# Kernel optimization log

Hardware: AMD Instinct MI355X
Metric: run time of the kernel (lower is better)

## Reference

```python
import jax, jax.numpy as jnp
import numpy as np

B, L, D, HW = 128, 512, 512, 512
NEG = -1e9


def _ff(x, weights):
    # feed-forward chain: relu(x @ W) per layer
    for w in weights:
        x = jax.nn.relu(jnp.matmul(x, w))
    return x


def _masked_softmax_flat(logits, mask):
    # softmax over the flattened last axis, masked entries excluded
    logits = jnp.where(mask > 0, logits, NEG)
    return jax.nn.softmax(logits, axis=-1)


def setup_inputs() -> dict:
    key = jax.random.key(0)
    ks = jax.random.split(key, 11)
    u = lambda k, shape: jax.random.uniform(k, shape, jnp.float32, -0.05, 0.05)
    return {
        "premise": jax.random.normal(ks[0], (B, L, D), jnp.float32),
        "hypothesis": jax.random.normal(ks[1], (B, L, D), jnp.float32),
        "premise_mask": jax.random.randint(ks[2], (B, L), 0, 2, jnp.int32),
        "hypothesis_mask": jax.random.randint(ks[3], (B, L), 0, 2, jnp.int32),
        "attend_w0": u(ks[4], (D, HW)),
        "attend_w1": u(ks[5], (HW, HW)),
        "compare_w0": u(ks[6], (2 * D, HW)),
        "compare_w1": u(ks[7], (HW, HW)),
        "aggregate_w0": u(ks[8], (2 * HW, HW)),
        "aggregate_w1": u(ks[9], (HW, HW)),
        "scorer": u(ks[10], (HW, 2)),
    }


def reference(premise, hypothesis, premise_mask, hypothesis_mask,
              attend_w0, attend_w1, compare_w0, compare_w1,
              aggregate_w0, aggregate_w1, scorer):
    pm = premise_mask.astype(premise.dtype)      # [B, P]
    hm = hypothesis_mask.astype(hypothesis.dtype)  # [B, H]
    p_emb = premise * pm[..., None]              # zero out masked words
    h_emb = hypothesis * hm[..., None]

    # Attend: project with shared F, score all pairs
    proj_p = _ff(p_emb, [attend_w0, attend_w1])  # [B, P, HW]
    proj_h = _ff(h_emb, [attend_w0, attend_w1])  # [B, H, HW]
    att = jnp.einsum('bpd,bhd->bph', proj_p, proj_h)  # [B, P, H]
    Bn, P, H = att.shape

    # Faithful to original: softmax over the *flattened* P*H axis with pairwise mask
    p2h_mask = (pm[:, :, None] * hm[:, None, :]).reshape(Bn, P * H)
    h2p_mask = (hm[:, :, None] * pm[:, None, :]).reshape(Bn, H * P)
    p2h = _masked_softmax_flat(att.reshape(Bn, P * H), p2h_mask).reshape(Bn, P, H)
    h2p = _masked_softmax_flat(jnp.swapaxes(att, 1, 2).reshape(Bn, H * P), h2p_mask).reshape(Bn, H, P)

    # Weighted sums (alignments)
    p2h_align = jnp.einsum('bph,bhd->bpd', p2h, h_emb)  # [B, P, D]
    h2p_align = jnp.einsum('bhp,bpd->bhd', h2p, p_emb)  # [B, H, D]

    # Compare with shared G
    compared_p = _ff(jnp.concatenate([p_emb, p2h_align], axis=-1), [compare_w0, compare_w1])
    compared_h = _ff(jnp.concatenate([h_emb, h2p_align], axis=-1), [compare_w0, compare_w1])

    # Aggregate with H, then score
    aggregated = jnp.concatenate([compared_p.sum(axis=1), compared_h.sum(axis=1)], axis=-1)  # [B, 2*HW]
    hidden = _ff(aggregated, [aggregate_w0, aggregate_w1])  # [B, HW]
    return jax.nn.softmax(jnp.matmul(hidden, scorer), axis=-1)  # [B, 2]
```

## Files before the change

kernel.cpp:

```cpp
#include <hip/hip_runtime.h>
#include <hip/hip_bf16.h>
#include <stdint.h>

typedef unsigned short u16;
typedef uint8_t u8;
typedef __bf16 bf16x8 __attribute__((ext_vector_type(8)));
typedef float f32x4 __attribute__((ext_vector_type(4)));

__device__ __forceinline__ u16 f2b(float f){
  uint32_t u = __float_as_uint(f);
  u = (u + 0x7fffu + ((u >> 16) & 1u)) >> 16;
  return (u16)u;
}
__device__ __forceinline__ float b2f(u16 u){
  return __uint_as_float(((uint32_t)u) << 16);
}
__device__ __forceinline__ uint32_t f2e4(float f){
  uint32_t u = __float_as_uint(f);
  uint32_t s = (u >> 24) & 0x80u;
  uint32_t a = u & 0x7fffffffu;
  if (a >= 0x43e00000u) return s | 0x7eu;
  if (a < 0x3c800000u){
    float v = __uint_as_float(a) * 512.0f + 12582912.0f;
    return s | (__float_as_uint(v) & 7u);
  }
  uint32_t t = a - (120u << 23);
  t += 0x7ffffu + ((t >> 20) & 1u);
  return s | (t >> 20);
}
__device__ __forceinline__ u16 e4b(uint32_t b){
  uint32_t s = (b & 0x80u) << 8;
  uint32_t e = (b >> 3) & 15u, m = b & 7u;
  if (e) return (u16)(s | ((e + 120u) << 7) | (m << 4));
  return (u16)(s | f2b((float)m * 0.001953125f));
}

typedef const void __attribute__((address_space(1))) gv_t;
typedef void __attribute__((address_space(3))) sv_t;

__device__ __forceinline__ void gload16(const void* g, void* l){
  __builtin_amdgcn_global_load_lds((gv_t*)g, (sv_t*)l, 16, 0, 0);
}

__global__ __launch_bounds__(256) void cnt_scan(const int* __restrict__ pm,
    const int* __restrict__ hm, int* __restrict__ pfx, int* __restrict__ cnts)
{
  int bs = blockIdx.x;
  const int* msk = (bs < 128) ? pm + bs*512 : hm + (bs-128)*512;
  __shared__ int sA[256], sB[256], fl[512];
  int t = threadIdx.x;
  int a = (msk[2*t] != 0), b = (msk[2*t+1] != 0);
  fl[2*t] = a; fl[2*t+1] = b;
  sA[t] = a + b;
  __syncthreads();
  int* cur = sA; int* nxt = sB;
  #pragma unroll
  for (int off = 1; off < 256; off <<= 1){
    int v = cur[t] + ((t >= off) ? cur[t-off] : 0);
    nxt[t] = v;
    __syncthreads();
    int* tmp = cur; cur = nxt; nxt = tmp;
  }
  int incl = cur[t];
  int excl = incl - fl[2*t] - fl[2*t+1];
  pfx[bs*512 + 2*t]     = excl;
  pfx[bs*512 + 2*t + 1] = excl + fl[2*t];
  if (t == 255) cnts[bs] = incl;
}

__global__ __launch_bounds__(256) void gscan_k(const int* __restrict__ cnts,
    int* __restrict__ gpfx, int* __restrict__ hloc)
{
  __shared__ int sA[256], sB[256];
  int t = threadIdx.x;
  int v0 = cnts[t];
  sA[t] = v0;
  __syncthreads();
  int* cur = sA; int* nxt = sB;
  #pragma unroll
  for (int off = 1; off < 256; off <<= 1){
    int v = cur[t] + ((t >= off) ? cur[t-off] : 0);
    nxt[t] = v;
    __syncthreads();
    int* tmp = cur; cur = nxt; nxt = tmp;
  }
  int incl = cur[t];
  gpfx[t] = incl - v0;
  if (t == 255) gpfx[256] = incl;
  __syncthreads();
  if (t >= 128) hloc[t - 128] = (incl - v0) - cur[127];
}

__global__ __launch_bounds__(256) void compact_copy(
    const float* __restrict__ prem, const float* __restrict__ hyp,
    const int* __restrict__ pm, const int* __restrict__ hm,
    const int* __restrict__ pfx, const int* __restrict__ gpfx,
    u8* __restrict__ embC8, int* __restrict__ rowMap)
{
  int blk = blockIdx.x;
  int bs = blk >> 2, qtr = blk & 3;
  const float* src = (bs < 128) ? prem + (long)bs*262144 : hyp + (long)(bs-128)*262144;
  const int*  msk = (bs < 128) ? pm + bs*512 : hm + (bs-128)*512;
  const int*  pf  = pfx + bs*512;
  long gbase = gpfx[bs];
  int t = threadIdx.x;
  for (int idx = t; idx < 128*32; idx += 256){
    int r = qtr*128 + (idx >> 5);
    if (msk[r] == 0) continue;
    int c = (idx & 31) * 16;
    int dr = pf[r];
    long g = gbase + dr;
    if ((idx & 31) == 0) rowMap[g] = bs*512 + dr;
    const float4* s4 = (const float4*)(src + (long)r*512 + c);
    float4 v0 = s4[0], v1 = s4[1], v2 = s4[2], v3 = s4[3];
    union { u8 o[16]; uint4 q; } u;
    u.o[0]=f2e4(v0.x); u.o[1]=f2e4(v0.y); u.o[2]=f2e4(v0.z); u.o[3]=f2e4(v0.w);
    u.o[4]=f2e4(v1.x); u.o[5]=f2e4(v1.y); u.o[6]=f2e4(v1.z); u.o[7]=f2e4(v1.w);
    u.o[8]=f2e4(v2.x); u.o[9]=f2e4(v2.y); u.o[10]=f2e4(v2.z); u.o[11]=f2e4(v2.w);
    u.o[12]=f2e4(v3.x); u.o[13]=f2e4(v3.y); u.o[14]=f2e4(v3.z); u.o[15]=f2e4(v3.w);
    *(uint4*)&embC8[g*512 + c] = u.q;
  }
}

__global__ void wtrans3_k(const float* __restrict__ W0, const float* __restrict__ W1,
                          const float* __restrict__ W2, u8* __restrict__ O0,
                          u8* __restrict__ O1, u8* __restrict__ O2){
  __shared__ float tile[32][33];
  const float* W = (blockIdx.z == 0) ? W0 : (blockIdx.z == 1 ? W1 : W2);
  u8* out        = (blockIdx.z == 0) ? O0 : (blockIdx.z == 1 ? O1 : O2);
  int c0 = blockIdx.x*32, r0 = blockIdx.y*32;
  int tx = threadIdx.x & 31, ty = threadIdx.x >> 5;
  #pragma unroll
  for (int i = 0; i < 4; ++i){
    int rr = ty + i*8;
    tile[rr][tx] = W[(long)(r0+rr)*512 + c0 + tx];
  }
  __syncthreads();
  #pragma unroll
  for (int i = 0; i < 4; ++i){
    int rr = ty + i*8;
    out[(long)(c0+rr)*512 + r0 + tx] = (u8)f2e4(tile[tx][rr]);
  }
}
__global__ void wtrans_k(const float* __restrict__ W, u8* __restrict__ out, int R, int C){
  __shared__ float tile[32][33];
  int c0 = blockIdx.x*32, r0 = blockIdx.y*32;
  int tx = threadIdx.x & 31, ty = threadIdx.x >> 5;
  #pragma unroll
  for (int i = 0; i < 4; ++i){
    int rr = ty + i*8;
    tile[rr][tx] = W[(long)(r0+rr)*C + c0 + tx];
  }
  __syncthreads();
  #pragma unroll
  for (int i = 0; i < 4; ++i){
    int rr = ty + i*8;
    out[(long)(c0+rr)*R + r0 + tx] = (u8)f2e4(tile[tx][rr]);
  }
}

__global__ __launch_bounds__(256) void btrans2(const u8* __restrict__ in,
    const int* __restrict__ gpfx, const int* __restrict__ cnts,
    u16* __restrict__ outP, u16* __restrict__ outH)
{
  __shared__ u16 tile[64][65];
  int z = blockIdx.z;
  long sbase = (long)gpfx[z] * 512;
  int cnt = cnts[z];
  int r0 = blockIdx.y*64;
  if (r0 >= ((cnt + 31) & ~31)) return;
  u16* dst = (z < 128) ? outP + (long)z*262144 : outH + (long)(z-128)*262144;
  int c0 = blockIdx.x*64;
  int t = threadIdx.x;
  int rr = t >> 3, cc = (t & 7)*8;
  #pragma unroll
  for (int pass = 0; pass < 2; ++pass){
    int r = rr + pass*32;
    uint2 v = {0, 0};
    if (r0 + r < cnt) v = *(const uint2*)&in[sbase + (long)(r0+r)*512 + c0+cc];
    const u8* vv = (const u8*)&v;
    #pragma unroll
    for (int j = 0; j < 8; ++j) tile[r][cc+j] = (r0 + r < cnt) ? e4b(vv[j]) : (u16)0;
  }
  __syncthreads();
  #pragma unroll
  for (int pass = 0; pass < 2; ++pass){
    int r = rr + pass*32;
    union { u16 o[8]; uint4 q; } u;
    #pragma unroll
    for (int j = 0; j < 8; ++j) u.o[j] = tile[cc+j][r];
    *(uint4*)&dst[(long)(c0+r)*512 + r0+cc] = u.q;
  }
}

template<int MODE, bool F8OUT>
__global__ __launch_bounds__(256) void gemm_nt(
    const u16* __restrict__ A0, const u16* __restrict__ Bt, void* __restrict__ Cout,
    const int* __restrict__ cnts, int cntMOff, int cntKOff,
    const int* __restrict__ goffA, const int* __restrict__ goffB, const int* __restrict__ goffC,
    float2* __restrict__ part,
    int N, int K, long sAb, long sBb, long sCb,
    int gyMask, int gyShift, int cpx)
{
  __shared__ u16 As[2][128*32];
  __shared__ u16 Bs[2][128*32];
  __shared__ float2 wred4[4];

  const int p = blockIdx.x;
  const int l = (p & 7)*cpx + (p >> 3);
  const int bx = l & 3;
  const int rest = l >> 2;
  const int by = rest & gyMask;
  const int bz = rest >> gyShift;
  const int ml = (by & 3) * 128;
  const int m0 = by*128, n0 = bx*128;
  const int t = threadIdx.x, lane = t & 63, wv = t >> 6;
  const int wm = wv >> 1, wn = wv & 1, r = lane & 15, q = lane >> 4;

  bool dead = (ml >= cnts[cntMOff + bz]);
  if (MODE == 3 && !dead) dead = (n0 >= cnts[128 + bz]);
  if (dead){
    if (MODE == 3 && t == 0) part[bz*16 + by*4 + bx] = float2{-3.0e38f, 0.f};
    return;
  }

  int Keff = K;
  if (cntKOff >= 0){
    int kc = cnts[cntKOff + bz];
    Keff = (kc + 31) & ~31;
    if (Keff < 32) Keff = 32;
  }
  const int nt = Keff >> 5;

  const u16* a0 = A0 + (goffA ? 0 : (long)bz*sAb);
  const long aro = (goffA ? goffA[bz] : 0);
  const u16* bt = Bt + (goffB ? 0 : (long)bz*sBb);
  const long bro = (goffB ? goffB[bz] : 0);

  f32x4 acc[4][4] = {};

  auto stage = [&](int buf, int k0){
    #pragma unroll
    for (int h = 0; h < 2; ++h){
      int c = t + h*256;
      int row = c >> 2;
      int qg = (c & 3) ^ ((row >> 1) & 3);
      int ks = k0 + qg*8;
      gload16(a0 + (aro + m0 + row)*512 + ks, &As[buf][c*8]);
      gload16(bt + (bro + n0 + row)*(long)K + ks, &Bs[buf][c*8]);
    }
  };

  stage(0, 0);
  __syncthreads();
  for (int it = 0; it < nt; ++it){
    const int cur = it & 1;
    if (it + 1 < nt) stage(cur ^ 1, (it + 1) << 5);
    bf16x8 af[4], bfr[4];
    #pragma unroll
    for (int mi = 0; mi < 4; ++mi){
      int row = wm*64 + mi*16 + r;
      af[mi] = *reinterpret_cast<const bf16x8*>(&As[cur][(row*4 + (q ^ ((row>>1)&3)))*8]);
    }
    #pragma unroll
    for (int ni = 0; ni < 4; ++ni){
      int row = wn*64 + ni*16 + r;
      bfr[ni] = *reinterpret_cast<const bf16x8*>(&Bs[cur][(row*4 + (q ^ ((row>>1)&3)))*8]);
    }
    #pragma unroll
    for (int mi = 0; mi < 4; ++mi)
      #pragma unroll
      for (int ni = 0; ni < 4; ++ni)
        acc[mi][ni] = __builtin_amdgcn_mfma_f32_16x16x32_bf16(af[mi], bfr[ni], acc[mi][ni], 0, 0, 0);
    __syncthreads();
  }

  if constexpr (MODE == 3){
    const int cp = cnts[bz], ch = cnts[128 + bz];
    int hc[4];
    #pragma unroll
    for (int ni = 0; ni < 4; ++ni) hc[ni] = (n0 + wn*64 + ni*16 + r) < ch;
    float tm = -3.0e38f, ts = 0.f;
    #pragma unroll
    for (int mi = 0; mi < 4; ++mi){
      #pragma unroll
      for (int i = 0; i < 4; ++i){
        int rr = m0 + wm*64 + mi*16 + q*4 + i;
        int prm = rr < cp;
        #pragma unroll
        for (int ni = 0; ni < 4; ++ni){
          float v = acc[mi][ni][i];
          int cc = n0 + wn*64 + ni*16 + r;
          ((u16*)Cout)[(long)bz*sCb + (long)rr*N + cc] = f2b(v);
          float lv = (prm && hc[ni]) ? v : -1.0e9f;
          float nm = fmaxf(tm, lv);
          ts = ts*__expf(tm - nm) + __expf(lv - nm);
          tm = nm;
        }
      }
    }
    #pragma unroll
    for (int d = 1; d < 64; d <<= 1){
      float om = __shfl_xor(tm, d), os = __shfl_xor(ts, d);
      float nm = fmaxf(tm, om);
      ts = ts*__expf(tm - nm) + os*__expf(om - nm);
      tm = nm;
    }
    if (lane == 0) wred4[wv] = float2{tm, ts};
    __syncthreads();
    if (t == 0){
      float m = wred4[0].x, s = wred4[0].y;
      #pragma unroll
      for (int w = 1; w < 4; ++w){
        float om = wred4[w].x, os = wred4[w].y, nm = fmaxf(m, om);
        s = s*__expf(m - nm) + os*__expf(om - nm); m = nm;
      }
      part[bz*16 + by*4 + bx] = float2{m, s};
    }
  } else {
    const long co = goffC[bz];
    const int lim = cnts[cntMOff + bz];
    #pragma unroll
    for (int mi = 0; mi < 4; ++mi){
      #pragma unroll
      for (int ni = 0; ni < 4; ++ni){
        int cc = n0 + wn*64 + ni*16 + r;
        #pragma unroll
        for (int i = 0; i < 4; ++i){
          int rr = m0 + wm*64 + mi*16 + q*4 + i;
          if (rr < lim){
            if (F8OUT) ((u8*)Cout)[(co + rr)*512 + cc] = (u8)f2e4(acc[mi][ni][i]);
            else       ((u16*)Cout)[(co + rr)*(long)N + cc] = f2b(acc[mi][ni][i]);
          }
        }
      }
    }
  }
}

template<int MODE, int OUTT, bool SPLIT>
__global__ __launch_bounds__(256) void gemm_p8(
    const u8* __restrict__ A0, const u8* __restrict__ AP1, const u8* __restrict__ AH1,
    const u8* __restrict__ Bt, void* __restrict__ Cout, float* __restrict__ aggOut,
    const int* __restrict__ gpfx, const int* __restrict__ rowMap, int K, int cpx)
{
  __shared__ __align__(16) u8 As[2][128*64];
  __shared__ __align__(16) u8 Bs[2][128*64];
  __shared__ float redbuf[3][128];

  int Mtot = gpfx[256]; if (Mtot > 81920) Mtot = 81920;
  const int Mp = SPLIT ? gpfx[128] : 0;
  const int p = blockIdx.x;
  const int l = (p & 7)*cpx + (p >> 3);
  const int bx = l & 3, by = l >> 2;
  const int m0 = by*128, n0 = bx*128;
  if (m0 >= Mtot) return;
  const int t = threadIdx.x, lane = t & 63, wv = t >> 6;
  const int wm = wv >> 1, wn = wv & 1, r = lane & 15, q = lane >> 4;

  f32x4 acc[4][4] = {};
  const int nt = K >> 6;

  auto stage = [&](int buf, int kb){
    #pragma unroll
    for (int h = 0; h < 2; ++h){
      int c = t + h*256;
      int row = c >> 2, pp = c & 3;
      int ks = kb + ((pp ^ ((row >> 1) & 3)) << 4);
      int gr = m0 + row;
      const u8* sA;
      if (SPLIT && ks >= 512)
        sA = (gr < Mp ? AP1 + (long)gr*512 : AH1 + (long)(gr - Mp)*512) + (ks - 512);
      else
        sA = A0 + (long)gr*512 + ks;
      gload16(sA, &As[buf][c*16]);
      gload16(Bt + (long)(n0 + row)*K + ks, &Bs[buf][c*16]);
    }
  };

  stage(0, 0);
  __syncthreads();
  for (int it = 0; it < nt; ++it){
    const int cur = it & 1;
    if (it + 1 < nt) stage(cur ^ 1, (it + 1) << 6);
    long afL[2][4], bfL[2][4];
    #pragma unroll
    for (int s = 0; s < 2; ++s){
      const int j = s*4 + q;
      #pragma unroll
      for (int mi = 0; mi < 4; ++mi){
        int row = wm*64 + mi*16 + r;
        afL[s][mi] = *(const long*)&As[cur][row*64 + ((((j>>1) ^ ((row>>1)&3))<<4) | ((j&1)<<3))];
      }
      #pragma unroll
      for (int ni = 0; ni < 4; ++ni){
        int row = wn*64 + ni*16 + r;
        bfL[s][ni] = *(const long*)&Bs[cur][row*64 + ((((j>>1) ^ ((row>>1)&3))<<4) | ((j&1)<<3))];
      }
    }
    #pragma unroll
    for (int s = 0; s < 2; ++s)
      #pragma unroll
      for (int mi = 0; mi < 4; ++mi)
        #pragma unroll
        for (int ni = 0; ni < 4; ++ni)
          acc[mi][ni] = __builtin_amdgcn_mfma_f32_16x16x32_fp8_fp8(afL[s][mi], bfL[s][ni], acc[mi][ni], 0, 0, 0);
    __syncthreads();
  }

  if constexpr (MODE == 0){
    #pragma unroll
    for (int mi = 0; mi < 4; ++mi){
      #pragma unroll
      for (int i = 0; i < 4; ++i){
        int gr = m0 + wm*64 + mi*16 + q*4 + i;
        if (gr >= Mtot) continue;
        #pragma unroll
        for (int ni = 0; ni < 4; ++ni){
          int cc = n0 + wn*64 + ni*16 + r;
          float v = fmaxf(acc[mi][ni][i], 0.f);
          if (OUTT == 0) ((u8*)Cout)[(long)gr*512 + cc] = (u8)f2e4(v);
          else           ((u16*)Cout)[(long)gr*512 + cc] = f2b(v);
        }
      }
    }
  } else {
    for (int i = t; i < 3*128; i += 256) ((float*)redbuf)[i] = 0.f;
    __syncthreads();
    const int side0 = rowMap[m0] >> 9;
    int slr[4][4];
    #pragma unroll
    for (int mi = 0; mi < 4; ++mi)
      #pragma unroll
      for (int i = 0; i < 4; ++i){
        int gr = m0 + wm*64 + mi*16 + q*4 + i;
        slr[mi][i] = (gr < Mtot) ? ((rowMap[gr] >> 9) - side0) : -1;
      }
    #pragma unroll
    for (int ni = 0; ni < 4; ++ni){
      float va = 0.f, vb = 0.f, vc = 0.f;
      #pragma unroll
      for (int mi = 0; mi < 4; ++mi)
        #pragma unroll
        for (int i = 0; i < 4; ++i){
          int sl = slr[mi][i];
          if (sl < 0) continue;
          float rv = fmaxf(acc[mi][ni][i], 0.f);
          if (sl == 0) va += rv; else if (sl == 1) vb += rv; else vc += rv;
        }
      int cc = wn*64 + ni*16 + r;
      if (va != 0.f) atomicAdd(&redbuf[0][cc], va);
      if (vb != 0.f) atomicAdd(&redbuf[1][cc], vb);
      if (vc != 0.f) atomicAdd(&redbuf[2][cc], vc);
    }
    __syncthreads();
    if (t < 128){
      #pragma unroll
      for (int sl = 0; sl < 3; ++sl){
        int side = side0 + sl;
        float v = redbuf[sl][t];
        if (side < 256 && v != 0.f) atomicAdd(&aggOut[(long)side*512 + t + n0], v);
      }
    }
  }
}

__global__ void sm_merge(const float2* __restrict__ part, float2* __restrict__ bms){
  int b = threadIdx.x;
  float m = -3.0e38f, s = 0.f;
  for (int i = 0; i < 16; ++i){
    float2 p = part[b*16 + i];
    float nm = fmaxf(m, p.x);
    s = s*__expf(m - nm) + p.y*__expf(p.x - nm);
    m = nm;
  }
  bms[b] = float2{m, 1.0f / s};
}

__global__ __launch_bounds__(256) void sm_write_t(const u16* __restrict__ att,
    const int* __restrict__ cnts, const int* __restrict__ gpfx, const int* __restrict__ hloc,
    const float2* __restrict__ bms, u16* __restrict__ p2h, u16* __restrict__ h2p)
{
  __shared__ u16 tile[64][65];
  int b = blockIdx.z, h0 = blockIdx.x*64, p0 = blockIdx.y*64;
  int cp = cnts[b], ch = cnts[128 + b];
  int cp32 = (cp + 31) & ~31, ch32 = (ch + 31) & ~31;
  bool needP = (p0 < cp) && (h0 < ch32);
  bool needH = (h0 < ch) && (p0 < cp32);
  if (!needP && !needH) return;
  float2 ms = bms[b];
  int t = threadIdx.x;
  int rr = t >> 3, cc = (t & 7)*8;
  long base = (long)b*262144;
  long pbase = gpfx[b];
  long hbase = hloc[b];
  #pragma unroll
  for (int pass = 0; pass < 2; ++pass){
    int pr = rr + pass*32;
    uint4 v = *(const uint4*)&att[base + (long)(p0+pr)*512 + h0+cc];
    const u16* vv = (const u16*)&v;
    int pa = (p0 + pr) < cp;
    union { u16 o[8]; uint4 q4; } u;
    #pragma unroll
    for (int j = 0; j < 8; ++j){
      float x = b2f(vv[j]);
      u.o[j] = (pa && (h0+cc+j) < ch) ? f2b(__expf(x - ms.x)*ms.y) : (u16)0;
    }
    if (pa) *(uint4*)&p2h[(pbase + p0+pr)*512 + h0+cc] = u.q4;
    #pragma unroll
    for (int j = 0; j < 8; ++j) tile[pr][cc+j] = u.o[j];
  }
  __syncthreads();
  #pragma unroll
  for (int pass = 0; pass < 2; ++pass){
    int hr = rr + pass*32;
    if (h0 + hr < ch){
      union { u16 o[8]; uint4 q4; } u;
      #pragma unroll
      for (int j = 0; j < 8; ++j) u.o[j] = tile[cc+j][hr];
      *(uint4*)&h2p[(hbase + h0+hr)*512 + p0+cc] = u.q4;
    }
  }
}

__global__ __launch_bounds__(256) void ff1_k(const float* __restrict__ agg,
    const float* __restrict__ g0, float* __restrict__ tt)
{
  __shared__ float xs[256];
  int b = blockIdx.y, kc = blockIdx.x, t = threadIdx.x;
  int kbase = kc*256;
  {
    int kk = kbase + t;
    xs[t] = (kk < 512) ? agg[b*512 + kk] : agg[(long)(128 + b)*512 + (kk - 512)];
  }
  __syncthreads();
  float ax = 0.f, ay = 0.f;
  #pragma unroll 4
  for (int k = 0; k < 256; ++k){
    float2 g = *(const float2*)(g0 + (long)(kbase + k)*512 + 2*t);
    ax += xs[k]*g.x; ay += xs[k]*g.y;
  }
  atomicAdd(&tt[b*512 + 2*t],     ax);
  atomicAdd(&tt[b*512 + 2*t + 1], ay);
}

__global__ __launch_bounds__(256) void ff2_k(const float* __restrict__ tt,
    const float* __restrict__ g1, float* __restrict__ x2)
{
  __shared__ float xs[128];
  int b = blockIdx.y, kc = blockIdx.x, t = threadIdx.x;
  int kbase = kc*128;
  if (t < 128) xs[t] = fmaxf(tt[b*512 + kbase + t], 0.f);
  __syncthreads();
  float ax = 0.f, ay = 0.f;
  #pragma unroll 4
  for (int k = 0; k < 128; ++k){
    float2 g = *(const float2*)(g1 + (long)(kbase + k)*512 + 2*t);
    ax += xs[k]*g.x; ay += xs[k]*g.y;
  }
  atomicAdd(&x2[b*512 + 2*t],     ax);
  atomicAdd(&x2[b*512 + 2*t + 1], ay);
}

__global__ __launch_bounds__(64) void score_k(const float* __restrict__ x2,
    const float* __restrict__ sc, float* __restrict__ out)
{
  int b = blockIdx.x, t = threadIdx.x;
  float s0 = 0.f, s1 = 0.f;
  for (int k = t; k < 512; k += 64){
    float v = fmaxf(x2[b*512 + k], 0.f);
    s0 += v*sc[2*k]; s1 += v*sc[2*k + 1];
  }
  #pragma unroll
  for (int d = 1; d < 64; d <<= 1){ s0 += __shfl_xor(s0, d); s1 += __shfl_xor(s1, d); }
  if (t == 0){
    float mm = fmaxf(s0, s1);
    float e0 = __expf(s0 - mm), e1 = __expf(s1 - mm);
    float inv = 1.f / (e0 + e1);
    out[2*b]     = e0*inv;
    out[2*b + 1] = e1*inv;
  }
}

extern "C" void kernel_launch(void* const* d_in, const int* in_sizes, int n_in,
                              void* d_out, int out_size, void* d_ws, size_t ws_size,
                              hipStream_t stream) {
  const float* premise    = (const float*)d_in[0];
  const float* hypothesis = (const float*)d_in[1];
  const int*   pm         = (const int*)d_in[2];
  const int*   hm         = (const int*)d_in[3];
  const float* w_a0       = (const float*)d_in[4];
  const float* w_a1       = (const float*)d_in[5];
  const float* w_c0       = (const float*)d_in[6];
  const float* w_c1       = (const float*)d_in[7];
  const float* w_g0       = (const float*)d_in[8];
  const float* w_g1       = (const float*)d_in[9];
  const float* w_sc       = (const float*)d_in[10];
  float* out = (float*)d_out;

  const size_t MB = 1ull << 20;
  if (ws_size < 456*MB) return;

  char* ws = (char*)d_ws;
  u8*  embC8 = (u8*)(ws + 0);
  u8*  t08   = (u8*)(ws + 40*MB);
  u8*  ap8   = (u8*)(ws + 40*MB);
  u8*  ah8   = (u8*)(ws + 60*MB);
  u16* proj  = (u16*)(ws + 80*MB);
  u8*  cmp8  = (u8*)(ws + 80*MB);
  u16* pT    = (u16*)(ws + 160*MB);
  u16* hT    = (u16*)(ws + 224*MB);
  u16* att_b = (u16*)(ws + 288*MB);
  u16* p2h   = (u16*)(ws + 352*MB);
  u16* h2p   = (u16*)(ws + 392*MB);
  u8*  wt_a0 = (u8*)(ws + 432*MB);
  u8*  wt_a1 = (u8*)(ws + 432*MB + 256*1024);
  u8*  wt_c1 = (u8*)(ws + 432*MB + 512*1024);
  u8*  wt_c0 = (u8*)(ws + 433*MB);
  float* agg = (float*)(ws + 434*MB);
  float* tt  = (float*)(ws + 434*MB + 512*1024);
  float* x2  = (float*)(ws + 434*MB + 768*1024);
  int*   pfx = (int*)(ws + 435*MB);
  int* rowMap= (int*)(ws + 436*MB);
  int*  gpfx = (int*)(ws + 437*MB);
  int*  hloc = (int*)(ws + 437*MB + 4096);
  int*  cnts = (int*)(ws + 437*MB + 8192);
  float2* part = (float2*)(ws + 437*MB + 12288);
  float2* bms  = (float2*)(ws + 437*MB + 32768);

  const long S = 262144;

  cnt_scan<<<256, 256, 0, stream>>>(pm, hm, pfx, cnts);
  gscan_k<<<1, 256, 0, stream>>>(cnts, gpfx, hloc);
  compact_copy<<<1024, 256, 0, stream>>>(premise, hypothesis, pm, hm, pfx, gpfx, embC8, rowMap);

  wtrans3_k<<<dim3(16,16,3), 256, 0, stream>>>(w_a0, w_a1, w_c1, wt_a0, wt_a1, wt_c1);
  wtrans_k<<<dim3(16,32), 256, 0, stream>>>(w_c0, wt_c0, 1024, 512);
  hipMemsetAsync(agg, 0, 256*512*sizeof(float), stream);
  hipMemsetAsync(tt,  0, 128*512*sizeof(float), stream);
  hipMemsetAsync(x2,  0, 128*512*sizeof(float), stream);

  gemm_p8<0,0,false><<<2112, 256, 0, stream>>>(embC8, nullptr, nullptr, wt_a0, t08, nullptr, gpfx, nullptr, 512, 264);
  gemm_p8<0,1,false><<<2112, 256, 0, stream>>>(t08, nullptr, nullptr, wt_a1, proj, nullptr, gpfx, nullptr, 512, 264);

  btrans2<<<dim3(8,8,256), 256, 0, stream>>>(embC8, gpfx, cnts, pT, hT);

  gemm_nt<3,false><<<2048, 256, 0, stream>>>(proj, proj, att_b, cnts, 0, -1,
      gpfx, gpfx + 128, nullptr, part, 512, 512, 0, 0, S, 3, 2, 256);

  sm_merge<<<1, 128, 0, stream>>>(part, bms);
  sm_write_t<<<dim3(8,8,128), 256, 0, stream>>>(att_b, cnts, gpfx, hloc, bms, p2h, h2p);

  gemm_nt<0,true><<<2048, 256, 0, stream>>>(p2h, hT, ap8, cnts, 0, 128,
      gpfx, nullptr, gpfx, nullptr, 512, 512, 0, S, 0, 3, 2, 256);
  gemm_nt<0,true><<<2048, 256, 0, stream>>>(h2p, pT, ah8, cnts, 128, 0,
      hloc, nullptr, hloc, nullptr, 512, 512, 0, S, 0, 3, 2, 256);

  gemm_p8<0,0,true><<<2112, 256, 0, stream>>>(embC8, ap8, ah8, wt_c0, cmp8, nullptr, gpfx, nullptr, 1024, 264);

  gemm_p8<2,0,false><<<2112, 256, 0, stream>>>(cmp8, nullptr, nullptr, wt_c1, nullptr, agg, gpfx, rowMap, 512, 264);

  ff1_k<<<dim3(4,128), 256, 0, stream>>>(agg, w_g0, tt);
  ff2_k<<<dim3(4,128), 256, 0, stream>>>(tt, w_g1, x2);
  score_k<<<128, 64, 0, stream>>>(x2, w_sc, out);
}
```

Baseline: 499.6 us.

## Compute alignment GEMMs in FP8 with a fused dual-side kernel

The softmax-weight outputs (p2h/h2p) and the transposed embeddings are now stored as FP8 e4m3 instead of bf16, and a new gemm_a8 kernel uses fp8 MFMA to compute both alignment products in one launch. The two previous gemm_nt launches are replaced, and halving the operand bytes cuts memory traffic and LDS footprint. Padding granularity moves from 32 to 64 rows to fit the K=64 tile. The trade-off is lower precision: softmax probabilities quantized to e4m3 lose many small values to subnormals or zero, which may hurt accuracy.

Result: faster. 453.6 us (-9.2%).

```diff
diff --git a/kernel.cpp b/kernel.cpp
--- a/kernel.cpp
+++ b/kernel.cpp
@@ -27,12 +27,6 @@
   uint32_t t = a - (120u << 23);
   t += 0x7ffffu + ((t >> 20) & 1u);
   return s | (t >> 20);
-}
-__device__ __forceinline__ u16 e4b(uint32_t b){
-  uint32_t s = (b & 0x80u) << 8;
-  uint32_t e = (b >> 3) & 15u, m = b & 7u;
-  if (e) return (u16)(s | ((e + 120u) << 7) | (m << 4));
-  return (u16)(s | f2b((float)m * 0.001953125f));
 }
 
 typedef const void __attribute__((address_space(1))) gv_t;
@@ -161,15 +155,15 @@
 
 __global__ __launch_bounds__(256) void btrans2(const u8* __restrict__ in,
     const int* __restrict__ gpfx, const int* __restrict__ cnts,
-    u16* __restrict__ outP, u16* __restrict__ outH)
-{
-  __shared__ u16 tile[64][65];
+    u8* __restrict__ outP, u8* __restrict__ outH)
+{
+  __shared__ u8 tile[64][72];
   int z = blockIdx.z;
   long sbase = (long)gpfx[z] * 512;
   int cnt = cnts[z];
   int r0 = blockIdx.y*64;
-  if (r0 >= ((cnt + 31) & ~31)) return;
-  u16* dst = (z < 128) ? outP + (long)z*262144 : outH + (long)(z-128)*262144;
+  if (r0 >= ((cnt + 63) & ~63)) return;
+  u8* dst = (z < 128) ? outP + (long)z*262144 : outH + (long)(z-128)*262144;
   int c0 = blockIdx.x*64;
   int t = threadIdx.x;
   int rr = t >> 3, cc = (t & 7)*8;
@@ -180,16 +174,16 @@
     if (r0 + r < cnt) v = *(const uint2*)&in[sbase + (long)(r0+r)*512 + c0+cc];
     const u8* vv = (const u8*)&v;
     #pragma unroll
-    for (int j = 0; j < 8; ++j) tile[r][cc+j] = (r0 + r < cnt) ? e4b(vv[j]) : (u16)0;
+    for (int j = 0; j < 8; ++j) tile[r][cc+j] = vv[j];
   }
   __syncthreads();
   #pragma unroll
   for (int pass = 0; pass < 2; ++pass){
     int r = rr + pass*32;
-    union { u16 o[8]; uint4 q; } u;
+    union { u8 o[8]; uint2 q2; } u;
     #pragma unroll
     for (int j = 0; j < 8; ++j) u.o[j] = tile[cc+j][r];
-    *(uint4*)&dst[(long)(c0+r)*512 + r0+cc] = u.q;
+    *(uint2*)&dst[(long)(c0+r)*512 + r0+cc] = u.q2;
   }
 }
 
@@ -465,6 +459,90 @@
   }
 }
 
+__global__ __launch_bounds__(256) void gemm_a8(
+    const u8* __restrict__ P2H, const u8* __restrict__ H2P,
+    const u8* __restrict__ PT8, const u8* __restrict__ HT8,
+    u8* __restrict__ AP, u8* __restrict__ AH,
+    const int* __restrict__ cnts, const int* __restrict__ gpfx, const int* __restrict__ hloc)
+{
+  __shared__ __align__(16) u8 As[2][128*64];
+  __shared__ __align__(16) u8 Bs[2][128*64];
+  const int p = blockIdx.x;
+  const int l = (p & 7)*512 + (p >> 3);
+  const int side = l >> 11;
+  const int r2 = l & 2047;
+  const int bx = r2 & 3, by = (r2 >> 2) & 3, bz = r2 >> 4;
+  const int Mlive = side ? cnts[128 + bz] : cnts[bz];
+  const int m0 = by*128, n0 = bx*128;
+  if (m0 >= Mlive) return;
+  const int Klive = side ? cnts[bz] : cnts[128 + bz];
+  int Keff = (Klive + 63) & ~63; if (Keff < 64) Keff = 64;
+  const int nt = Keff >> 6;
+  const long abase = side ? (long)hloc[bz] : (long)gpfx[bz];
+  const u8* A0 = (side ? H2P : P2H) + abase*512;
+  const u8* Bt = (side ? PT8 : HT8) + (long)bz*262144;
+  u8* Cp = (side ? AH : AP) + abase*512;
+  const int t = threadIdx.x, lane = t & 63, wv = t >> 6;
+  const int wm = wv >> 1, wn = wv & 1, r = lane & 15, q = lane >> 4;
+
+  f32x4 acc[4][4] = {};
+
+  auto stage = [&](int buf, int kb){
+    #pragma unroll
+    for (int h = 0; h < 2; ++h){
+      int c = t + h*256;
+      int row = c >> 2, pp = c & 3;
+      int ks = kb + ((pp ^ ((row >> 1) & 3)) << 4);
+      gload16(A0 + (long)(m0 + row)*512 + ks, &As[buf][c*16]);
+      gload16(Bt + (long)(n0 + row)*512 + ks, &Bs[buf][c*16]);
+    }
+  };
+
+  stage(0, 0);
+  __syncthreads();
+  for (int it = 0; it < nt; ++it){
+    const int cur = it & 1;
+    if (it + 1 < nt) stage(cur ^ 1, (it + 1) << 6);
+    long afL[2][4], bfL[2][4];
+    #pragma unroll
+    for (int s = 0; s < 2; ++s){
+      const int j = s*4 + q;
+      #pragma unroll
+      for (int mi = 0; mi < 4; ++mi){
+        int row = wm*64 + mi*16 + r;
+        afL[s][mi] = *(const long*)&As[cur][row*64 + ((((j>>1) ^ ((row>>1)&3))<<4) | ((j&1)<<3))];
+      }
+      #pragma unroll
+      for (int ni = 0; ni < 4; ++ni){
+        int row = wn*64 + ni*16 + r;
+        bfL[s][ni] = *(const long*)&Bs[cur][row*64 + ((((j>>1) ^ ((row>>1)&3))<<4) | ((j&1)<<3))];
+      }
+    }
+    #pragma unroll
+    for (int s = 0; s < 2; ++s)
+      #pragma unroll
+      for (int mi = 0; mi < 4; ++mi)
+        #pragma unroll
+        for (int ni = 0; ni < 4; ++ni)
+          acc[mi][ni] = __builtin_amdgcn_mfma_f32_16x16x32_fp8_fp8(afL[s][mi], bfL[s][ni], acc[mi][ni], 0, 0, 0);
+    __syncthreads();
+  }
+
+  #pragma unroll
+  for (int mi = 0; mi < 4; ++mi){
+    #pragma unroll
+    for (int i = 0; i < 4; ++i){
+      int lr = m0 + wm*64 + mi*16 + q*4 + i;
+      if (lr >= Mlive) continue;
+      #pragma unroll
+      for (int ni = 0; ni < 4; ++ni){
+        int cc = n0 + wn*64 + ni*16 + r;
+        Cp[(long)lr*512 + cc] = (u8)f2e4(acc[mi][ni][i]);
+      }
+    }
+  }
+}
+
 __global__ void sm_merge(const float2* __restrict__ part, float2* __restrict__ bms){
   int b = threadIdx.x;
   float m = -3.0e38f, s = 0.f;
@@ -479,14 +557,14 @@
 
 __global__ __launch_bounds__(256) void sm_write_t(const u16* __restrict__ att,
     const int* __restrict__ cnts, const int* __restrict__ gpfx, const int* __restrict__ hloc,
-    const float2* __restrict__ bms, u16* __restrict__ p2h, u16* __restrict__ h2p)
-{
-  __shared__ u16 tile[64][65];
+    const float2* __restrict__ bms, u8* __restrict__ p2h, u8* __restrict__ h2p)
+{
+  __shared__ u8 tile[64][72];
   int b = blockIdx.z, h0 = blockIdx.x*64, p0 = blockIdx.y*64;
   int cp = cnts[b], ch = cnts[128 + b];
-  int cp32 = (cp + 31) & ~31, ch32 = (ch + 31) & ~31;
-  bool needP = (p0 < cp) && (h0 < ch32);
-  bool needH = (h0 < ch) && (p0 < cp32);
+  int cp64 = (cp + 63) & ~63, ch64 = (ch + 63) & ~63;
+  bool needP = (p0 < cp) && (h0 < ch64);
+  bool needH = (h0 < ch) && (p0 < cp64);
   if (!needP && !needH) return;
   float2 ms = bms[b];
   int t = threadIdx.x;
@@ -500,13 +578,13 @@
     uint4 v = *(const uint4*)&att[base + (long)(p0+pr)*512 + h0+cc];
     const u16* vv = (const u16*)&v;
     int pa = (p0 + pr) < cp;
-    union { u16 o[8]; uint4 q4; } u;
+    union { u8 o[8]; uint2 q2; } u;
     #pragma unroll
     for (int j = 0; j < 8; ++j){
       float x = b2f(vv[j]);
-      u.o[j] = (pa && (h0+cc+j) < ch) ? f2b(__expf(x - ms.x)*ms.y) : (u16)0;
-    }
-    if (pa) *(uint4*)&p2h[(pbase + p0+pr)*512 + h0+cc] = u.q4;
+      u.o[j] = (pa && (h0+cc+j) < ch) ? (u8)f2e4(__expf(x - ms.x)*ms.y) : (u8)0;
+    }
+    if (pa) *(uint2*)&p2h[(pbase + p0+pr)*512 + h0+cc] = u.q2;
     #pragma unroll
     for (int j = 0; j < 8; ++j) tile[pr][cc+j] = u.o[j];
   }
@@ -515,10 +593,10 @@
   for (int pass = 0; pass < 2; ++pass){
     int hr = rr + pass*32;
     if (h0 + hr < ch){
-      union { u16 o[8]; uint4 q4; } u;
+      union { u8 o[8]; uint2 q2; } u;
       #pragma unroll
       for (int j = 0; j < 8; ++j) u.o[j] = tile[cc+j][hr];
-      *(uint4*)&h2p[(hbase + h0+hr)*512 + p0+cc] = u.q4;
+      *(uint2*)&h2p[(hbase + h0+hr)*512 + p0+cc] = u.q2;
     }
   }
 }
@@ -608,11 +686,11 @@
   u8*  ah8   = (u8*)(ws + 60*MB);
   u16* proj  = (u16*)(ws + 80*MB);
   u8*  cmp8  = (u8*)(ws + 80*MB);
-  u16* pT    = (u16*)(ws + 160*MB);
-  u16* hT    = (u16*)(ws + 224*MB);
+  u8*  pT8   = (u8*)(ws + 160*MB);
+  u8*  hT8   = (u8*)(ws + 200*MB);
   u16* att_b = (u16*)(ws + 288*MB);
-  u16* p2h   = (u16*)(ws + 352*MB);
-  u16* h2p   = (u16*)(ws + 392*MB);
+  u8*  p2h8  = (u8*)(ws + 352*MB);
+  u8*  h2p8  = (u8*)(ws + 372*MB);
   u8*  wt_a0 = (u8*)(ws + 432*MB);
   u8*  wt_a1 = (u8*)(ws + 432*MB + 256*1024);
   u8*  wt_c1 = (u8*)(ws + 432*MB + 512*1024);
@@ -643,18 +721,15 @@
   gemm_p8<0,0,false><<<2112, 256, 0, stream>>>(embC8, nullptr, nullptr, wt_a0, t08, nullptr, gpfx, nullptr, 512, 264);
   gemm_p8<0,1,false><<<2112, 256, 0, stream>>>(t08, nullptr, nullptr, wt_a1, proj, nullptr, gpfx, nullptr, 512, 264);
 
-  btrans2<<<dim3(8,8,256), 256, 0, stream>>>(embC8, gpfx, cnts, pT, hT);
+  btrans2<<<dim3(8,8,256), 256, 0, stream>>>(embC8, gpfx, cnts, pT8, hT8);
 
   gemm_nt<3,false><<<2048, 256, 0, stream>>>(proj, proj, att_b, cnts, 0, -1,
       gpfx, gpfx + 128, nullptr, part, 512, 512, 0, 0, S, 3, 2, 256);
 
   sm_merge<<<1, 128, 0, stream>>>(part, bms);
-  sm_write_t<<<dim3(8,8,128), 256, 0, stream>>>(att_b, cnts, gpfx, hloc, bms, p2h, h2p);
-
-  gemm_nt<0,true><<<2048, 256, 0, stream>>>(p2h, hT, ap8, cnts, 0, 128,
-      gpfx, nullptr, gpfx, nullptr, 512, 512, 0, S, 0, 3, 2, 256);
-  gemm_nt<0,true><<<2048, 256, 0, stream>>>(h2p, pT, ah8, cnts, 128, 0,
-      hloc, nullptr, hloc, nullptr, 512, 512, 0, S, 0, 3, 2, 256);
+  sm_write_t<<<dim3(8,8,128), 256, 0, stream>>>(att_b, cnts, gpfx, hloc, bms, p2h8, h2p8);
+
+  gemm_a8<<<4096, 256, 0, stream>>>(p2h8, h2p8, pT8, hT8, ap8, ah8, cnts, gpfx, hloc);
 
   gemm_p8<0,0,true><<<2112, 256, 0, stream>>>(embC8, ap8, ah8, wt_c0, cmp8, nullptr, gpfx, nullptr, 1024, 264);
 
```
